# Kernel optimization log

Measured on AMD Instinct MI355X. Metric: run time of the kernel, lower is better.

Reference implementation:

```python
import jax, jax.numpy as jnp
import numpy as np

N = 50000
E = 400000  # bidirectional: second half is reverse of first half
D = 128
T = 3
EPS = 1e-09


def apply_lambda(x, log_dt, log_lambda_real, lambda_imag, one_minus=False):
    # lambda_complex = exp((-exp(log_lambda_real) + 1j*lambda_imag) * dt)
    dt = jnp.exp(log_dt)
    mag = jnp.exp(-jnp.exp(log_lambda_real) * dt)          # |lambda| [D//2]
    mag = jnp.where(one_minus, 1.0 - mag, mag)
    phase = lambda_imag * dt                                # angle (cos/sin are wrap-invariant)
    c, s = jnp.cos(phase), jnp.sin(phase)
    xp = x.reshape(x.shape[:-1] + (-1, 2))                  # [..., D//2, 2]
    xr = (c * xp[..., 0] - s * xp[..., 1]) * mag
    xi = (s * xp[..., 0] + c * xp[..., 1]) * mag
    return jnp.stack((xr, xi), axis=-1).reshape(x.shape)


def setup_inputs() -> dict:
    key = jax.random.key(0)
    kx, ke1, ke2, k1, k2, k3, k4 = jax.random.split(key, 7)
    x = jax.random.normal(kx, (N, D), dtype=jnp.float32)
    a = jax.random.randint(ke1, (E // 2,), 0, N)
    b = jax.random.randint(ke2, (E // 2,), 0, N)
    edge_index = jnp.stack([jnp.concatenate([a, b]), jnp.concatenate([b, a])], axis=0)
    hidden = D + D
    scale1 = 1.0 / np.sqrt(D)
    scale2 = 1.0 / np.sqrt(hidden)
    return {
        "x": x,
        "edge_index": edge_index,
        "log_dt": jnp.asarray(np.log(0.1), dtype=jnp.float32),
        "log_lambda_real": jnp.full((D // 2,), np.log(0.5), dtype=jnp.float32),
        "lambda_imag": jnp.arange(D // 2, dtype=jnp.float32) * np.pi,
        "W1": jax.random.uniform(k1, (D, hidden), jnp.float32, -scale1, scale1),
        "W2": jax.random.uniform(k2, (D, hidden), jnp.float32, -scale1, scale1),
        "Wp": jax.random.uniform(k3, (hidden, D), jnp.float32, -scale2, scale2),
        "bp": jax.random.uniform(k4, (D,), jnp.float32, -scale2, scale2),
    }


def reference(x, edge_index, log_dt, log_lambda_real, lambda_imag, W1, W2, Wp, bp):
    x_in = x  # dim_in == dim_out -> residual from pre-MLP input
    # MLP: silu(x W1) * (x W2) -> proj
    h = jax.nn.silu(x @ W1) * (x @ W2)
    x = h @ Wp + bp

    lam = lambda v, om=False: apply_lambda(v, log_dt, log_lambda_real, lambda_imag, om)
    src, dst = edge_index[0], edge_index[1]

    deg = jax.ops.segment_sum(jnp.ones((E,), x.dtype), src, num_segments=N)  # [N]
    M = x[src]                                                              # [E, D]
    m = jax.ops.segment_sum(M, dst, num_segments=N)                         # [N, D]

    for _ in range(T):
        M_ji = jnp.concatenate((M[E // 2:], M[:E // 2]), axis=0)            # reverse-edge message
        x_e = x[src]
        deg_e = deg[src][:, None]
        M = jnp.where(deg_e == 1,
                      x_e,
                      lam(x_e, True) + lam(m[src] - M_ji) / (deg_e - 1 + EPS))
        m = jax.ops.segment_sum(M, dst, num_segments=N)

    out = jnp.where(deg[:, None] == 0, x, lam(x, True) + lam(m) / (deg[:, None] + EPS))
    out = jax.nn.relu(out)  # dropout p=0 (eval)
    return x_in + out
```

## Files before the change

### kernel.cpp

```cpp
#include <hip/hip_runtime.h>

#define EPSF 1e-9f

typedef __bf16 bf16x8 __attribute__((ext_vector_type(8)));
typedef float  f32x4  __attribute__((ext_vector_type(4)));
typedef unsigned short ushort_t;
typedef unsigned int uint_t;
typedef ushort_t us8 __attribute__((ext_vector_type(8)));

__device__ __forceinline__ float2 cmul(float cr, float ci, float2 v) {
    return make_float2(cr * v.x - ci * v.y, ci * v.x + cr * v.y);
}

__device__ __forceinline__ ushort_t f2bf(float f) {
    unsigned int u = __float_as_uint(f);
    u += 0x7FFFu + ((u >> 16) & 1u);
    return (ushort_t)(u >> 16);
}

__device__ __forceinline__ float2 bfu2(uint_t u) {
    return make_float2(__uint_as_float(u << 16), __uint_as_float(u & 0xFFFF0000u));
}
__device__ __forceinline__ uint_t packbf(float2 v) {
    return ((uint_t)f2bf(v.y) << 16) | (uint_t)f2bf(v.x);
}

__global__ void k_lamtab(const float* __restrict__ ldt, const float* __restrict__ llr,
                         const float* __restrict__ lim, float* __restrict__ tab) {
    int p = threadIdx.x;
    if (p >= 64) return;
    float dt  = expf(ldt[0]);
    float mag = expf(-expf(llr[p]) * dt);
    float ph  = lim[p] * dt;
    float c = cosf(ph), s = sinf(ph);
    float m2 = mag * mag, m3 = m2 * mag;
    float c2 = c * c - s * s, s2 = 2.f * c * s;
    float c3 = c2 * c - s2 * s, s3 = s2 * c + c2 * s;
    tab[p]        = c * mag;          tab[64 + p]  = s * mag;
    tab[128 + p]  = c * (1.f - mag);  tab[192 + p] = s * (1.f - mag);
    tab[256 + p]  = c2 * m2;          tab[320 + p] = s2 * m2;
    tab[384 + p]  = c3 * m3;          tab[448 + p] = s3 * m3;
}

__global__ void k_prepw(const float* __restrict__ w, ushort_t* __restrict__ wb,
                        int ncols, int nsteps, int total) {
    int tid = blockIdx.x * blockDim.x + threadIdx.x;
    if (tid >= total) return;
    int l  = tid & 63;
    int s  = (tid >> 6) % nsteps;
    int nt = tid / (64 * nsteps);
    int col = nt * 16 + (l & 15);
    int kb  = s * 32 + (l >> 4) * 8;
    us8 d;
#pragma unroll
    for (int j = 0; j < 8; ++j) d[j] = f2bf(w[(size_t)(kb + j) * ncols + col]);
    *(us8*)(wb + (size_t)tid * 8) = d;
}

__global__ void __launch_bounds__(256)
k_mlpf(const float* __restrict__ x, const ushort_t* __restrict__ wb1,
       const ushort_t* __restrict__ wb2, const ushort_t* __restrict__ wpb,
       const float* __restrict__ bp, ushort_t* __restrict__ xpb, int Mt) {
    __shared__ ushort_t hs[2][4096];
    const int wid = threadIdx.x >> 6, l = threadIdx.x & 63;
    const int mt0 = blockIdx.x * 2;
    const bool has1 = (mt0 + 1) < Mt;
    const int llo = l & 15, lhi = l >> 4;

    bf16x8 af[2][4];
#pragma unroll
    for (int m = 0; m < 2; ++m) {
        int mt = (m == 1 && !has1) ? mt0 : (mt0 + m);
        const float* xr = x + (size_t)(mt * 16 + llo) * 128 + lhi * 8;
#pragma unroll
        for (int s = 0; s < 4; ++s) {
            float4 v0 = *(const float4*)(xr + s * 32);
            float4 v1 = *(const float4*)(xr + s * 32 + 4);
            us8 d;
            d[0] = f2bf(v0.x); d[1] = f2bf(v0.y); d[2] = f2bf(v0.z); d[3] = f2bf(v0.w);
            d[4] = f2bf(v1.x); d[5] = f2bf(v1.y); d[6] = f2bf(v1.z); d[7] = f2bf(v1.w);
            af[m][s] = *(bf16x8*)&d;
        }
    }

    const bf16x8* B1 = (const bf16x8*)wb1;
    const bf16x8* B2 = (const bf16x8*)wb2;
    const bf16x8* BP = (const bf16x8*)wpb;
    const f32x4 zero = {0.f, 0.f, 0.f, 0.f};

#pragma unroll
    for (int j = 0; j < 4; ++j) {
        int nt = wid * 4 + j;
        bf16x8 b1[4], b2[4];
#pragma unroll
        for (int s = 0; s < 4; ++s) {
            b1[s] = B1[(nt * 4 + s) * 64 + l];
            b2[s] = B2[(nt * 4 + s) * 64 + l];
        }
#pragma unroll
        for (int m = 0; m < 2; ++m) {
            f32x4 a1 = zero, a2 = zero;
#pragma unroll
            for (int s = 0; s < 4; ++s) {
                a1 = __builtin_amdgcn_mfma_f32_16x16x32_bf16(af[m][s], b1[s], a1, 0, 0, 0);
                a2 = __builtin_amdgcn_mfma_f32_16x16x32_bf16(af[m][s], b2[s], a2, 0, 0, 0);
            }
#pragma unroll
            for (int i = 0; i < 4; ++i) {
                float g = a1[i];
                float hv = (g / (1.f + __expf(-g))) * a2[i];
                int r = 4 * lhi + i;
                int byte = (r << 9) + ((nt * 16 + llo) << 1);
                byte ^= (r & 7) << 4;
                hs[m][byte >> 1] = f2bf(hv);
            }
        }
    }
    __syncthreads();

#pragma unroll
    for (int j = 0; j < 2; ++j) {
        int nt3 = wid * 2 + j;
        f32x4 acc0 = zero, acc1 = zero;
#pragma unroll
        for (int sg = 0; sg < 8; ++sg) {
            bf16x8 bw = BP[(nt3 * 8 + sg) * 64 + l];
            int byte = (llo << 9) + (sg << 6) + (lhi << 4);
            byte ^= (llo & 7) << 4;
            bf16x8 h0 = *(const bf16x8*)((const char*)hs[0] + byte);
            acc0 = __builtin_amdgcn_mfma_f32_16x16x32_bf16(h0, bw, acc0, 0, 0, 0);
            bf16x8 h1 = *(const bf16x8*)((const char*)hs[1] + byte);
            acc1 = __builtin_amdgcn_mfma_f32_16x16x32_bf16(h1, bw, acc1, 0, 0, 0);
        }
        float bpv = bp[nt3 * 16 + llo];
        {
            const int row0 = mt0 * 16;
#pragma unroll
            for (int i = 0; i < 4; ++i) {
                int r = row0 + 4 * lhi + i;
                xpb[(size_t)r * 128 + nt3 * 16 + llo] = f2bf(acc0[i] + bpv);
            }
        }
        if (has1) {
            const int row0 = (mt0 + 1) * 16;
#pragma unroll
            for (int i = 0; i < 4; ++i) {
                int r = row0 + 4 * lhi + i;
                xpb[(size_t)r * 128 + nt3 * 16 + llo] = f2bf(acc1[i] + bpv);
            }
        }
    }
}

__global__ void k_hist(const int* __restrict__ ei, int E, int* __restrict__ cnt) {
    int e = blockIdx.x * blockDim.x + threadIdx.x;
    if (e < E) atomicAdd(&cnt[ei[E + e]], 1);
}

__global__ void __launch_bounds__(256)
k_scanA(const int* __restrict__ cnt, int N, int* __restrict__ bsum) {
    __shared__ int s[256];
    int t = threadIdx.x;
    int i = blockIdx.x * 256 + t;
    int v = (i < N) ? cnt[i] : 0;
    s[t] = v;
    __syncthreads();
#pragma unroll
    for (int d = 128; d > 0; d >>= 1) {
        if (t < d) s[t] += s[t + d];
        __syncthreads();
    }
    if (t == 0) bsum[blockIdx.x] = s[0];
}

__global__ void __launch_bounds__(1024)
k_scanB(const int* __restrict__ bsum, int NB, int* __restrict__ bpre,
        int* __restrict__ offN) {
    __shared__ int s[1024];
    int t = threadIdx.x;
    int v = (t < NB) ? bsum[t] : 0;
    s[t] = v;
    __syncthreads();
    for (int d = 1; d < 1024; d <<= 1) {
        int u = (t >= d) ? s[t - d] : 0;
        __syncthreads();
        s[t] += u;
        __syncthreads();
    }
    if (t < NB) bpre[t] = s[t] - v;
    if (t == NB - 1) *offN = s[t];
}

__global__ void __launch_bounds__(256)
k_scanC(const int* __restrict__ cnt, int N, const int* __restrict__ bpre,
        int* __restrict__ off, int* __restrict__ cursor, float* __restrict__ bv) {
    __shared__ int s[256];
    int t = threadIdx.x;
    int i = blockIdx.x * 256 + t;
    int v = (i < N) ? cnt[i] : 0;
    s[t] = v;
    __syncthreads();
    for (int d = 1; d < 256; d <<= 1) {
        int u = (t >= d) ? s[t - d] : 0;
        __syncthreads();
        s[t] += u;
        __syncthreads();
    }
    if (i < N) {
        int excl = bpre[blockIdx.x] + s[t] - v;
        off[i] = excl;
        cursor[i] = excl;
        bv[i] = (v > 1) ? (-1.f / ((float)v - 1.f + EPSF)) : 0.f;
    }
}

__global__ void k_fill(const int* __restrict__ ei, int E, const float* __restrict__ bv,
                       int* __restrict__ cursor, uint2* __restrict__ csrb) {
    int e = blockIdx.x * blockDim.x + threadIdx.x;
    if (e < E) {
        int s = ei[e], d = ei[E + e];
        int p = atomicAdd(&cursor[d], 1);
        csrb[p] = make_uint2((uint_t)s, __float_as_uint(bv[s]));
    }
}

__global__ void __launch_bounds__(256)
k_passA(const ushort_t* __restrict__ xpb, const uint2* __restrict__ eb,
        const int* __restrict__ off, const float* __restrict__ tab,
        ushort_t* __restrict__ Xbb, ushort_t* __restrict__ a1b, int N) {
    int tid = blockIdx.x * blockDim.x + threadIdx.x;
    int v = tid >> 6, l = tid & 63;
    if (v >= N) return;
    int beg = off[v], end = off[v + 1];
    float2 m0 = make_float2(0.f, 0.f), xb = make_float2(0.f, 0.f);
    const uint_t* tb = (const uint_t*)xpb;
    int k = beg;
    for (; k + 3 < end; k += 4) {
        uint2 e0 = eb[k], e1 = eb[k + 1], e2 = eb[k + 2], e3 = eb[k + 3];
        uint_t u0 = tb[(size_t)e0.x * 64 + l];
        uint_t u1 = tb[(size_t)e1.x * 64 + l];
        uint_t u2 = tb[(size_t)e2.x * 64 + l];
        uint_t u3 = tb[(size_t)e3.x * 64 + l];
        float b0 = __uint_as_float(e0.y), b1 = __uint_as_float(e1.y);
        float b2 = __uint_as_float(e2.y), b3 = __uint_as_float(e3.y);
        float2 t0 = bfu2(u0), t1 = bfu2(u1), t2 = bfu2(u2), t3 = bfu2(u3);
        m0.x += (t0.x + t1.x) + (t2.x + t3.x);
        m0.y += (t0.y + t1.y) + (t2.y + t3.y);
        xb.x += b0 * t0.x + b1 * t1.x + b2 * t2.x + b3 * t3.x;
        xb.y += b0 * t0.y + b1 * t1.y + b2 * t2.y + b3 * t3.y;
    }
    for (; k < end; ++k) {
        uint2 e0 = eb[k];
        float2 t0 = bfu2(tb[(size_t)e0.x * 64 + l]);
        float b0 = __uint_as_float(e0.y);
        m0.x += t0.x; m0.y += t0.y;
        xb.x += b0 * t0.x; xb.y += b0 * t0.y;
    }
    ((uint_t*)Xbb)[(size_t)v * 64 + l] = packbf(xb);
    float2 xv = bfu2(tb[(size_t)v * 64 + l]);
    int dg = end - beg;
    float L1r = tab[l], L1i = tab[64 + l], O1r = tab[128 + l], O1i = tab[192 + l];
    float Q = 1.f / ((float)dg - 1.f + EPSF);
    float2 t1 = cmul(O1r, O1i, xv);
    float2 t2 = cmul(L1r, L1i, m0);
    float2 a = make_float2(t1.x + Q * t2.x, t1.y + Q * t2.y);
    if (dg == 1) a = xv;
    ((uint_t*)a1b)[(size_t)v * 64 + l] = packbf(a);
}

__global__ void __launch_bounds__(256)
k_passB(const ushort_t* __restrict__ xpb, const ushort_t* __restrict__ a1b,
        const uint2* __restrict__ eb, const int* __restrict__ off,
        const float* __restrict__ tab, ushort_t* __restrict__ ab1b,
        float* __restrict__ Bv, float* __restrict__ B2v,
        ushort_t* __restrict__ a2b, int N) {
    int tid = blockIdx.x * blockDim.x + threadIdx.x;
    int v = tid >> 6, l = tid & 63;
    if (v >= N) return;
    int beg = off[v], end = off[v + 1];
    float2 A1 = make_float2(0.f, 0.f), ab = make_float2(0.f, 0.f);
    float Bs = 0.f, B2s = 0.f;
    const uint_t* tb = (const uint_t*)a1b;
    int k = beg;
    for (; k + 3 < end; k += 4) {
        uint2 e0 = eb[k], e1 = eb[k + 1], e2 = eb[k + 2], e3 = eb[k + 3];
        uint_t u0 = tb[(size_t)e0.x * 64 + l];
        uint_t u1 = tb[(size_t)e1.x * 64 + l];
        uint_t u2 = tb[(size_t)e2.x * 64 + l];
        uint_t u3 = tb[(size_t)e3.x * 64 + l];
        float b0 = __uint_as_float(e0.y), b1 = __uint_as_float(e1.y);
        float b2 = __uint_as_float(e2.y), b3 = __uint_as_float(e3.y);
        float2 t0 = bfu2(u0), t1 = bfu2(u1), t2 = bfu2(u2), t3 = bfu2(u3);
        A1.x += (t0.x + t1.x) + (t2.x + t3.x);
        A1.y += (t0.y + t1.y) + (t2.y + t3.y);
        ab.x += b0 * t0.x + b1 * t1.x + b2 * t2.x + b3 * t3.x;
        ab.y += b0 * t0.y + b1 * t1.y + b2 * t2.y + b3 * t3.y;
        Bs += (b0 + b1) + (b2 + b3);
        B2s += (b0 * b0 + b1 * b1) + (b2 * b2 + b3 * b3);
    }
    for (; k < end; ++k) {
        uint2 e0 = eb[k];
        float2 t0 = bfu2(tb[(size_t)e0.x * 64 + l]);
        float b0 = __uint_as_float(e0.y);
        A1.x += t0.x; A1.y += t0.y;
        ab.x += b0 * t0.x; ab.y += b0 * t0.y;
        Bs += b0; B2s += b0 * b0;
    }
    ((uint_t*)ab1b)[(size_t)v * 64 + l] = packbf(ab);
    if (l == 0) { Bv[v] = Bs; B2v[v] = B2s; }
    float2 xv = bfu2(((const uint_t*)xpb)[(size_t)v * 64 + l]);
    int dg = end - beg;
    float L1r = tab[l], L1i = tab[64 + l], O1r = tab[128 + l], O1i = tab[192 + l];
    float2 lx = cmul(L1r, L1i, xv);
    float2 m1 = make_float2(A1.x + Bs * lx.x, A1.y + Bs * lx.y);
    float Q = 1.f / ((float)dg - 1.f + EPSF);
    float2 t1 = cmul(O1r, O1i, xv);
    float2 lm = cmul(L1r, L1i, m1);
    float2 a = make_float2(t1.x + Q * lm.x, t1.y + Q * lm.y);
    if (dg == 1) a = xv;
    ((uint_t*)a2b)[(size_t)v * 64 + l] = packbf(a);
}

__global__ void __launch_bounds__(256)
k_passC(const ushort_t* __restrict__ xpb, const ushort_t* __restrict__ a2b,
        const ushort_t* __restrict__ a1b, const ushort_t* __restrict__ Xbb,
        const float* __restrict__ bv, const float* __restrict__ Bv,
        const uint2* __restrict__ eb, const int* __restrict__ off,
        const float* __restrict__ tab, ushort_t* __restrict__ a3b, int N) {
    int tid = blockIdx.x * blockDim.x + threadIdx.x;
    int v = tid >> 6, l = tid & 63;
    if (v >= N) return;
    int beg = off[v], end = off[v + 1];
    float2 A2 = make_float2(0.f, 0.f);
    const uint_t* tb = (const uint_t*)a2b;
    int k = beg;
    for (; k + 3 < end; k += 4) {
        uint2 e0 = eb[k], e1 = eb[k + 1], e2 = eb[k + 2], e3 = eb[k + 3];
        float2 t0 = bfu2(tb[(size_t)e0.x * 64 + l]);
        float2 t1 = bfu2(tb[(size_t)e1.x * 64 + l]);
        float2 t2 = bfu2(tb[(size_t)e2.x * 64 + l]);
        float2 t3 = bfu2(tb[(size_t)e3.x * 64 + l]);
        A2.x += (t0.x + t1.x) + (t2.x + t3.x);
        A2.y += (t0.y + t1.y) + (t2.y + t3.y);
    }
    for (; k < end; ++k) {
        float2 t0 = bfu2(tb[(size_t)eb[k].x * 64 + l]);
        A2.x += t0.x; A2.y += t0.y;
    }
    float2 xv  = bfu2(((const uint_t*)xpb)[(size_t)v * 64 + l]);
    float2 a1v = bfu2(((const uint_t*)a1b)[(size_t)v * 64 + l]);
    float2 Xbv = bfu2(((const uint_t*)Xbb)[(size_t)v * 64 + l]);
    int dg = end - beg;
    float Bs = Bv[v], bs = bv[v];
    float L1r = tab[l], L1i = tab[64 + l], O1r = tab[128 + l], O1i = tab[192 + l];
    float L2r = tab[256 + l], L2i = tab[320 + l];
    float2 la1 = cmul(L1r, L1i, a1v);
    float2 lxb = cmul(L2r, L2i, Xbv);
    float2 m2 = make_float2(A2.x + Bs * la1.x + bs * lxb.x,
                            A2.y + Bs * la1.y + bs * lxb.y);
    float Q = 1.f / ((float)dg - 1.f + EPSF);
    float2 t1 = cmul(O1r, O1i, xv);
    float2 lm = cmul(L1r, L1i, m2);
    float2 a = make_float2(t1.x + Q * lm.x, t1.y + Q * lm.y);
    if (dg == 1) a = xv;
    ((uint_t*)a3b)[(size_t)v * 64 + l] = packbf(a);
}

__global__ void __launch_bounds__(256)
k_passD(const float* __restrict__ xin, const ushort_t* __restrict__ xpb,
        const ushort_t* __restrict__ a3b, const ushort_t* __restrict__ a2b,
        const ushort_t* __restrict__ ab1b, const float* __restrict__ bv,
        const float* __restrict__ Bv, const float* __restrict__ B2v,
        const uint2* __restrict__ eb, const int* __restrict__ off,
        const float* __restrict__ tab, float* __restrict__ out, int N) {
    int tid = blockIdx.x * blockDim.x + threadIdx.x;
    int v = tid >> 6, l = tid & 63;
    if (v >= N) return;
    int beg = off[v], end = off[v + 1];
    float2 A3 = make_float2(0.f, 0.f);
    const uint_t* tb = (const uint_t*)a3b;
    int k = beg;
    for (; k + 3 < end; k += 4) {
        uint2 e0 = eb[k], e1 = eb[k + 1], e2 = eb[k + 2], e3 = eb[k + 3];
        float2 t0 = bfu2(tb[(size_t)e0.x * 64 + l]);
        float2 t1 = bfu2(tb[(size_t)e1.x * 64 + l]);
        float2 t2 = bfu2(tb[(size_t)e2.x * 64 + l]);
        float2 t3 = bfu2(tb[(size_t)e3.x * 64 + l]);
        A3.x += (t0.x + t1.x) + (t2.x + t3.x);
        A3.y += (t0.y + t1.y) + (t2.y + t3.y);
    }
    for (; k < end; ++k) {
        float2 t0 = bfu2(tb[(size_t)eb[k].x * 64 + l]);
        A3.x += t0.x; A3.y += t0.y;
    }
    size_t o = (size_t)v * 128 + 2 * l;
    float2 xv  = bfu2(((const uint_t*)xpb)[(size_t)v * 64 + l]);
    float2 a2v = bfu2(((const uint_t*)a2b)[(size_t)v * 64 + l]);
    float2 Abv = bfu2(((const uint_t*)ab1b)[(size_t)v * 64 + l]);
    int dg = end - beg;
    float Bs = Bv[v], bs = bv[v], B2s = B2v[v];
    float L1r = tab[l], L1i = tab[64 + l], O1r = tab[128 + l], O1i = tab[192 + l];
    float L2r = tab[256 + l], L2i = tab[320 + l];
    float L3r = tab[384 + l], L3i = tab[448 + l];
    float2 la2 = cmul(L1r, L1i, a2v);
    float2 lab = cmul(L2r, L2i, Abv);
    float2 lx3 = cmul(L3r, L3i, xv);
    float bB2 = bs * B2s;
    float2 m3 = make_float2(A3.x + Bs * la2.x + bs * lab.x + bB2 * lx3.x,
                            A3.y + Bs * la2.y + bs * lab.y + bB2 * lx3.y);
    float2 g;
    if (dg == 0) {
        g = xv;
    } else {
        float inv = 1.f / ((float)dg + EPSF);
        float2 t1 = cmul(O1r, O1i, xv);
        float2 lm = cmul(L1r, L1i, m3);
        g = make_float2(t1.x + lm.x * inv, t1.y + lm.y * inv);
    }
    float2 xi = *(const float2*)&xin[o];
    float2 res = make_float2(xi.x + fmaxf(g.x, 0.f), xi.y + fmaxf(g.y, 0.f));
    *(float2*)&out[o] = res;
}

extern "C" void kernel_launch(void* const* d_in, const int* in_sizes, int n_in,
                              void* d_out, int out_size, void* d_ws, size_t ws_size,
                              hipStream_t stream) {
    const float* x   = (const float*)d_in[0];
    const int*   ei  = (const int*)d_in[1];
    const float* ldt = (const float*)d_in[2];
    const float* llr = (const float*)d_in[3];
    const float* lim = (const float*)d_in[4];
    const float* W1  = (const float*)d_in[5];
    const float* W2  = (const float*)d_in[6];
    const float* Wp  = (const float*)d_in[7];
    const float* bp  = (const float*)d_in[8];
    float* out = (float*)d_out;

    const int N = in_sizes[0] / 128;
    const int E = in_sizes[1] / 2;
    const size_t nd = (size_t)N * 128;
    const int Mt = (N + 15) / 16;
    const int Mt2 = (Mt + 1) / 2;
    const int NB = (N + 255) / 256;

    ushort_t* xpb  = (ushort_t*)d_ws;
    ushort_t* a1b  = xpb + nd;
    ushort_t* a2b  = a1b + nd;
    ushort_t* a3b  = a2b + nd;
    ushort_t* Xbb  = a3b + nd;
    ushort_t* ab1b = Xbb + nd;

    int*   cnt    = (int*)(ab1b + nd);
    int*   off    = cnt + N;
    int*   cursor = off + N + 4;
    float* bv     = (float*)(cursor + N);
    float* Bv     = bv + N;
    float* B2v    = Bv + N;
    float* tab    = B2v + N;
    int*   bsum   = (int*)(tab + 512);
    int*   bpre   = bsum + NB;
    uint2* csrb   = (uint2*)(bpre + NB + (NB & 1));
    ushort_t* wb1 = (ushort_t*)(csrb + E);
    ushort_t* wb2 = wb1 + 32768;
    ushort_t* wpb = wb2 + 32768;

    const int nodeBlocks = (int)(((size_t)N * 64 + 255) / 256);
    const int eBlocks    = (E + 255) / 256;

    hipMemsetAsync(cnt, 0, (size_t)N * sizeof(int), stream);
    k_lamtab<<<1, 64, 0, stream>>>(ldt, llr, lim, tab);

    k_prepw<<<16, 256, 0, stream>>>(W1, wb1, 256, 4, 16 * 4 * 64);
    k_prepw<<<16, 256, 0, stream>>>(W2, wb2, 256, 4, 16 * 4 * 64);
    k_prepw<<<16, 256, 0, stream>>>(Wp, wpb, 128, 8, 8 * 8 * 64);
    k_mlpf<<<Mt2, 256, 0, stream>>>(x, wb1, wb2, wpb, bp, xpb, Mt);

    k_hist<<<eBlocks, 256, 0, stream>>>(ei, E, cnt);
    k_scanA<<<NB, 256, 0, stream>>>(cnt, N, bsum);
    k_scanB<<<1, 1024, 0, stream>>>(bsum, NB, bpre, &off[N]);
    k_scanC<<<NB, 256, 0, stream>>>(cnt, N, bpre, off, cursor, bv);
    k_fill<<<eBlocks, 256, 0, stream>>>(ei, E, bv, cursor, csrb);

    k_passA<<<nodeBlocks, 256, 0, stream>>>(xpb, csrb, off, tab, Xbb, a1b, N);
    k_passB<<<nodeBlocks, 256, 0, stream>>>(xpb, a1b, csrb, off, tab, ab1b, Bv, B2v, a2b, N);
    k_passC<<<nodeBlocks, 256, 0, stream>>>(xpb, a2b, a1b, Xbb, bv, Bv, csrb, off, tab, a3b, N);
    k_passD<<<nodeBlocks, 256, 0, stream>>>(x, xpb, a3b, a2b, ab1b, bv, Bv, B2v, csrb, off, tab, out, N);
}
```

Before: 218.1 us.

## Merge setup kernels and unroll edge gather loops by eight

Replaces the memset and lambda-table kernel with one init kernel that zeroes the counts and builds the table. The three weight-prep launches become one. This cuts five setup operations down to two launches. The four per-node gather passes now unroll by 8 instead of 4, so more independent gathers are in flight per wavefront; this costs more registers and leaves more edges for the scalar tail when degrees are low (average degree is about 8).

After: 239.8 us. 1.1x slower.

```diff
diff --git a/kernel.cpp b/kernel.cpp
--- a/kernel.cpp
+++ b/kernel.cpp
@@ -25,27 +25,35 @@
     return ((uint_t)f2bf(v.y) << 16) | (uint_t)f2bf(v.x);
 }
 
-__global__ void k_lamtab(const float* __restrict__ ldt, const float* __restrict__ llr,
-                         const float* __restrict__ lim, float* __restrict__ tab) {
-    int p = threadIdx.x;
-    if (p >= 64) return;
-    float dt  = expf(ldt[0]);
-    float mag = expf(-expf(llr[p]) * dt);
-    float ph  = lim[p] * dt;
-    float c = cosf(ph), s = sinf(ph);
-    float m2 = mag * mag, m3 = m2 * mag;
-    float c2 = c * c - s * s, s2 = 2.f * c * s;
-    float c3 = c2 * c - s2 * s, s3 = s2 * c + c2 * s;
-    tab[p]        = c * mag;          tab[64 + p]  = s * mag;
-    tab[128 + p]  = c * (1.f - mag);  tab[192 + p] = s * (1.f - mag);
-    tab[256 + p]  = c2 * m2;          tab[320 + p] = s2 * m2;
-    tab[384 + p]  = c3 * m3;          tab[448 + p] = s3 * m3;
-}
-
-__global__ void k_prepw(const float* __restrict__ w, ushort_t* __restrict__ wb,
-                        int ncols, int nsteps, int total) {
+__global__ void k_init(const float* __restrict__ ldt, const float* __restrict__ llr,
+                       const float* __restrict__ lim, float* __restrict__ tab,
+                       int* __restrict__ cnt, int N) {
+    int i = blockIdx.x * blockDim.x + threadIdx.x;
+    if (i < N) cnt[i] = 0;
+    if (blockIdx.x == 0 && threadIdx.x < 64) {
+        int p = threadIdx.x;
+        float dt  = expf(ldt[0]);
+        float mag = expf(-expf(llr[p]) * dt);
+        float ph  = lim[p] * dt;
+        float c = cosf(ph), s = sinf(ph);
+        float m2 = mag * mag, m3 = m2 * mag;
+        float c2 = c * c - s * s, s2 = 2.f * c * s;
+        float c3 = c2 * c - s2 * s, s3 = s2 * c + c2 * s;
+        tab[p]        = c * mag;          tab[64 + p]  = s * mag;
+        tab[128 + p]  = c * (1.f - mag);  tab[192 + p] = s * (1.f - mag);
+        tab[256 + p]  = c2 * m2;          tab[320 + p] = s2 * m2;
+        tab[384 + p]  = c3 * m3;          tab[448 + p] = s3 * m3;
+    }
+}
+
+__global__ void k_prepw3(const float* __restrict__ W1, const float* __restrict__ W2,
+                         const float* __restrict__ Wp, ushort_t* __restrict__ wb1,
+                         ushort_t* __restrict__ wb2, ushort_t* __restrict__ wpb) {
     int tid = blockIdx.x * blockDim.x + threadIdx.x;
-    if (tid >= total) return;
+    const float* w; ushort_t* wb; int ncols, nsteps;
+    if (tid < 4096)       { w = W1; wb = wb1; ncols = 256; nsteps = 4; }
+    else if (tid < 8192)  { tid -= 4096; w = W2; wb = wb2; ncols = 256; nsteps = 4; }
+    else                  { tid -= 8192; w = Wp; wb = wpb; ncols = 128; nsteps = 8; }
     int l  = tid & 63;
     int s  = (tid >> 6) % nsteps;
     int nt = tid / (64 * nsteps);
@@ -235,19 +243,20 @@
     float2 m0 = make_float2(0.f, 0.f), xb = make_float2(0.f, 0.f);
     const uint_t* tb = (const uint_t*)xpb;
     int k = beg;
-    for (; k + 3 < end; k += 4) {
-        uint2 e0 = eb[k], e1 = eb[k + 1], e2 = eb[k + 2], e3 = eb[k + 3];
-        uint_t u0 = tb[(size_t)e0.x * 64 + l];
-        uint_t u1 = tb[(size_t)e1.x * 64 + l];
-        uint_t u2 = tb[(size_t)e2.x * 64 + l];
-        uint_t u3 = tb[(size_t)e3.x * 64 + l];
-        float b0 = __uint_as_float(e0.y), b1 = __uint_as_float(e1.y);
-        float b2 = __uint_as_float(e2.y), b3 = __uint_as_float(e3.y);
-        float2 t0 = bfu2(u0), t1 = bfu2(u1), t2 = bfu2(u2), t3 = bfu2(u3);
-        m0.x += (t0.x + t1.x) + (t2.x + t3.x);
-        m0.y += (t0.y + t1.y) + (t2.y + t3.y);
-        xb.x += b0 * t0.x + b1 * t1.x + b2 * t2.x + b3 * t3.x;
-        xb.y += b0 * t0.y + b1 * t1.y + b2 * t2.y + b3 * t3.y;
+    for (; k + 7 < end; k += 8) {
+        uint2 e[8];
+#pragma unroll
+        for (int j = 0; j < 8; ++j) e[j] = eb[k + j];
+        uint_t u[8];
+#pragma unroll
+        for (int j = 0; j < 8; ++j) u[j] = tb[(size_t)e[j].x * 64 + l];
+#pragma unroll
+        for (int j = 0; j < 8; ++j) {
+            float b = __uint_as_float(e[j].y);
+            float2 t0 = bfu2(u[j]);
+            m0.x += t0.x; m0.y += t0.y;
+            xb.x += b * t0.x; xb.y += b * t0.y;
+        }
     }
     for (; k < end; ++k) {
         uint2 e0 = eb[k];
@@ -282,21 +291,21 @@
     float Bs = 0.f, B2s = 0.f;
     const uint_t* tb = (const uint_t*)a1b;
     int k = beg;
-    for (; k + 3 < end; k += 4) {
-        uint2 e0 = eb[k], e1 = eb[k + 1], e2 = eb[k + 2], e3 = eb[k + 3];
-        uint_t u0 = tb[(size_t)e0.x * 64 + l];
-        uint_t u1 = tb[(size_t)e1.x * 64 + l];
-        uint_t u2 = tb[(size_t)e2.x * 64 + l];
-        uint_t u3 = tb[(size_t)e3.x * 64 + l];
-        float b0 = __uint_as_float(e0.y), b1 = __uint_as_float(e1.y);
-        float b2 = __uint_as_float(e2.y), b3 = __uint_as_float(e3.y);
-        float2 t0 = bfu2(u0), t1 = bfu2(u1), t2 = bfu2(u2), t3 = bfu2(u3);
-        A1.x += (t0.x + t1.x) + (t2.x + t3.x);
-        A1.y += (t0.y + t1.y) + (t2.y + t3.y);
-        ab.x += b0 * t0.x + b1 * t1.x + b2 * t2.x + b3 * t3.x;
-        ab.y += b0 * t0.y + b1 * t1.y + b2 * t2.y + b3 * t3.y;
-        Bs += (b0 + b1) + (b2 + b3);
-        B2s += (b0 * b0 + b1 * b1) + (b2 * b2 + b3 * b3);
+    for (; k + 7 < end; k += 8) {
+        uint2 e[8];
+#pragma unroll
+        for (int j = 0; j < 8; ++j) e[j] = eb[k + j];
+        uint_t u[8];
+#pragma unroll
+        for (int j = 0; j < 8; ++j) u[j] = tb[(size_t)e[j].x * 64 + l];
+#pragma unroll
+        for (int j = 0; j < 8; ++j) {
+            float b = __uint_as_float(e[j].y);
+            float2 t0 = bfu2(u[j]);
+            A1.x += t0.x; A1.y += t0.y;
+            ab.x += b * t0.x; ab.y += b * t0.y;
+            Bs += b; B2s += b * b;
+        }
     }
     for (; k < end; ++k) {
         uint2 e0 = eb[k];
@@ -334,14 +343,15 @@
     float2 A2 = make_float2(0.f, 0.f);
     const uint_t* tb = (const uint_t*)a2b;
     int k = beg;
-    for (; k + 3 < end; k += 4) {
-        uint2 e0 = eb[k], e1 = eb[k + 1], e2 = eb[k + 2], e3 = eb[k + 3];
-        float2 t0 = bfu2(tb[(size_t)e0.x * 64 + l]);
-        float2 t1 = bfu2(tb[(size_t)e1.x * 64 + l]);
-        float2 t2 = bfu2(tb[(size_t)e2.x * 64 + l]);
-        float2 t3 = bfu2(tb[(size_t)e3.x * 64 + l]);
-        A2.x += (t0.x + t1.x) + (t2.x + t3.x);
-        A2.y += (t0.y + t1.y) + (t2.y + t3.y);
+    for (; k + 7 < end; k += 8) {
+        uint_t u[8];
+#pragma unroll
+        for (int j = 0; j < 8; ++j) u[j] = tb[(size_t)eb[k + j].x * 64 + l];
+#pragma unroll
+        for (int j = 0; j < 8; ++j) {
+            float2 t0 = bfu2(u[j]);
+            A2.x += t0.x; A2.y += t0.y;
+        }
     }
     for (; k < end; ++k) {
         float2 t0 = bfu2(tb[(size_t)eb[k].x * 64 + l]);
@@ -380,14 +390,15 @@
     float2 A3 = make_float2(0.f, 0.f);
     const uint_t* tb = (const uint_t*)a3b;
     int k = beg;
-    for (; k + 3 < end; k += 4) {
-        uint2 e0 = eb[k], e1 = eb[k + 1], e2 = eb[k + 2], e3 = eb[k + 3];
-        float2 t0 = bfu2(tb[(size_t)e0.x * 64 + l]);
-        float2 t1 = bfu2(tb[(size_t)e1.x * 64 + l]);
-        float2 t2 = bfu2(tb[(size_t)e2.x * 64 + l]);
-        float2 t3 = bfu2(tb[(size_t)e3.x * 64 + l]);
-        A3.x += (t0.x + t1.x) + (t2.x + t3.x);
-        A3.y += (t0.y + t1.y) + (t2.y + t3.y);
+    for (; k + 7 < end; k += 8) {
+        uint_t u[8];
+#pragma unroll
+        for (int j = 0; j < 8; ++j) u[j] = tb[(size_t)eb[k + j].x * 64 + l];
+#pragma unroll
+        for (int j = 0; j < 8; ++j) {
+            float2 t0 = bfu2(u[j]);
+            A3.x += t0.x; A3.y += t0.y;
+        }
     }
     for (; k < end; ++k) {
         float2 t0 = bfu2(tb[(size_t)eb[k].x * 64 + l]);
@@ -467,12 +478,9 @@
     const int nodeBlocks = (int)(((size_t)N * 64 + 255) / 256);
     const int eBlocks    = (E + 255) / 256;
 
-    hipMemsetAsync(cnt, 0, (size_t)N * sizeof(int), stream);
-    k_lamtab<<<1, 64, 0, stream>>>(ldt, llr, lim, tab);
-
-    k_prepw<<<16, 256, 0, stream>>>(W1, wb1, 256, 4, 16 * 4 * 64);
-    k_prepw<<<16, 256, 0, stream>>>(W2, wb2, 256, 4, 16 * 4 * 64);
-    k_prepw<<<16, 256, 0, stream>>>(Wp, wpb, 128, 8, 8 * 8 * 64);
+    k_init<<<NB, 256, 0, stream>>>(ldt, llr, lim, tab, cnt, N);
+
+    k_prepw3<<<48, 256, 0, stream>>>(W1, W2, Wp, wb1, wb2, wpb);
     k_mlpf<<<Mt2, 256, 0, stream>>>(x, wb1, wb2, wpb, bp, xpb, Mt);
 
     k_hist<<<eBlocks, 256, 0, stream>>>(ei, E, cnt);
```
